# Kernel tuning notes

Measured on AMD Instinct MI355X. Metric: run time of the kernel, lower is better.

Reference implementation:

```python
import jax, jax.numpy as jnp
import numpy as np

H1, H, OUT, T = 512, 2048, 1024, 4096

def setup_inputs() -> dict:
    key = jax.random.key(0)
    ks = jax.random.split(key, 20)
    s = 0.02
    return {
        "input": jax.random.normal(ks[0], (1, OUT), jnp.float32),
        "hidden": jax.random.normal(ks[1], (1, 1, H), jnp.float32) * 0.1,
        "encoder_outputs": jax.random.normal(ks[2], (T, H), jnp.float32),
        "prenet_w": jax.random.normal(ks[3], (H1, OUT), jnp.float32) * s,
        "prenet_b": jnp.zeros((H1,), jnp.float32),
        "prenet2_w": jax.random.normal(ks[4], (H, H1), jnp.float32) * s,
        "prenet2_b": jnp.zeros((H,), jnp.float32),
        "attn1_w": jax.random.normal(ks[5], (H, H), jnp.float32) * s,
        "attn2_w": jax.random.normal(ks[6], (H, H), jnp.float32) * s,
        "attn3_w": jax.random.normal(ks[7], (1, H), jnp.float32) * s,
        "gru_w_ih": jax.random.normal(ks[8], (3 * H, 2 * H), jnp.float32) * s,
        "gru_w_hh": jax.random.normal(ks[9], (3 * H, H), jnp.float32) * s,
        "gru_b_ih": jnp.zeros((3 * H,), jnp.float32),
        "gru_b_hh": jnp.zeros((3 * H,), jnp.float32),
        "lin_w": jax.random.normal(ks[10], (OUT, H), jnp.float32) * s,
        "lin_b": jnp.zeros((OUT,), jnp.float32),
    }

def reference(input, hidden, encoder_outputs, prenet_w, prenet_b, prenet2_w,
              prenet2_b, attn1_w, attn2_w, attn3_w, gru_w_ih, gru_w_hh,
              gru_b_ih, gru_b_hh, lin_w, lin_b):
    # prenet MLP (dropout in eval mode = identity)
    em6 = jax.nn.relu(jax.nn.relu(input @ prenet_w.T + prenet_b) @ prenet2_w.T + prenet2_b)  # [1,H]
    # Bahdanau additive attention
    way = em6 @ attn1_w.T                                 # [1,H]
    uah = encoder_outputs @ attn2_w.T                     # [T,H]
    beta = jnp.tanh(way + uah)                            # [T,H] (broadcast = expand_as)
    gamma = beta @ attn3_w.T                              # [T,1]
    attn_weights = jax.nn.softmax(gamma.T, axis=1)        # [1,T]
    attn_applied = attn_weights @ encoder_outputs         # [1,H]
    # single-step GRU (PyTorch gate order: r, z, n)
    x = jnp.concatenate([em6, attn_applied], axis=1)      # [1,2H]
    h0 = hidden[0]                                        # [1,H]
    gi = x @ gru_w_ih.T + gru_b_ih                        # [1,3H]
    gh = h0 @ gru_w_hh.T + gru_b_hh                       # [1,3H]
    i_r, i_z, i_n = jnp.split(gi, 3, axis=1)
    h_r, h_z, h_n = jnp.split(gh, 3, axis=1)
    r = jax.nn.sigmoid(i_r + h_r)
    z = jax.nn.sigmoid(i_z + h_z)
    n = jnp.tanh(i_n + r * h_n)
    h_new = (1.0 - z) * n + z * h0                        # [1,H]
    out = jax.nn.softmax(h_new @ lin_w.T + lin_b, axis=1) # [1,OUT]
    return out, h_new[None], attn_weights
```

## Files before the change

### kernel.cpp

```cpp
#include <hip/hip_runtime.h>
#include <hip/hip_bf16.h>

typedef __bf16 bf16x8 __attribute__((ext_vector_type(8)));
typedef __bf16 bf16x4 __attribute__((ext_vector_type(4)));
typedef float f32x4 __attribute__((ext_vector_type(4)));

#define H1 512
#define H 2048
#define OUTN 1024
#define T 4096

__global__ __launch_bounds__(256) void matvec_k(
    const float* __restrict__ W, const float* __restrict__ x,
    const float* __restrict__ b, float* __restrict__ out,
    int R, int K, int relu)
{
    int row = blockIdx.x * 4 + (threadIdx.x >> 6);
    int lane = threadIdx.x & 63;
    if (row >= R) return;
    const float* Wr = W + (size_t)row * K;
    float s = 0.f;
    for (int k = lane * 4; k < K; k += 256) {
        float4 w4 = *(const float4*)(Wr + k);
        float4 x4 = *(const float4*)(x + k);
        s += w4.x * x4.x + w4.y * x4.y + w4.z * x4.z + w4.w * x4.w;
    }
    #pragma unroll
    for (int m = 32; m; m >>= 1) s += __shfl_xor(s, m, 64);
    if (lane == 0) {
        if (b) s += b[row];
        if (relu) s = fmaxf(s, 0.f);
        out[row] = s;
    }
}

__global__ __launch_bounds__(256) void cvt_sw_k(
    const float* __restrict__ E, const float* __restrict__ W2,
    __bf16* __restrict__ dst)
{
    int c = blockIdx.x * 256 + threadIdx.x;
    int row = c >> 8;
    int kc = c & 255;
    const float* src = (row < T) ? (E + (size_t)row * H + kc * 8)
                                 : (W2 + (size_t)(row - T) * H + kc * 8);
    float4 a = *(const float4*)src;
    float4 b = *(const float4*)(src + 4);
    bf16x8 v = {(__bf16)a.x, (__bf16)a.y, (__bf16)a.z, (__bf16)a.w,
                (__bf16)b.x, (__bf16)b.y, (__bf16)b.z, (__bf16)b.w};
    int grp = kc >> 3, cc = kc & 7;
    int sw = cc ^ (row & 7);
    *(bf16x8*)(dst + (size_t)row * H + grp * 64 + sw * 8) = v;
}

__global__ __launch_bounds__(256, 4) void gamma_gemm5(
    const __bf16* __restrict__ Asw,
    const __bf16* __restrict__ Bsw,
    const float* __restrict__ way, const float* __restrict__ a3,
    float* __restrict__ gamma)
{
    __shared__ __attribute__((aligned(16))) __bf16 As[128][64];
    __shared__ __attribute__((aligned(16))) __bf16 Bs[64][64];
    __shared__ float wayS[64], a3S[64];

    const int tb = blockIdx.x, hb = blockIdx.y;
    const int tid = threadIdx.x, lane = tid & 63, wid = tid >> 6;
    const int wr = wid >> 1, wc = wid & 1;
    if (tid < 64) { wayS[tid] = way[hb * 64 + tid]; a3S[tid] = a3[hb * 64 + tid]; }

    const int K = 2048;
    const __bf16* Ap = Asw + (size_t)(tb * 128) * K;
    const __bf16* Bp = Bsw + (size_t)(hb * 64) * K;

    f32x4 acc[4][2] = {};
    const int rl = lane & 15;
    const int kg = (lane >> 4) * 8;

    for (int t = 0; t < 32; ++t) {
        const int k0 = t * 64;
        #pragma unroll
        for (int j = 0; j < 4; ++j) {
            int c = tid + j * 256;
            int row_ = c >> 3, cc_ = c & 7;
            const __bf16* sA_ = Ap + (size_t)row_ * K + k0 + cc_ * 8;
            __builtin_amdgcn_global_load_lds(
                (const __attribute__((address_space(1))) void*)sA_,
                (__attribute__((address_space(3))) void*)((char*)&As[0][0] + c * 16),
                16, 0, 0);
        }
        #pragma unroll
        for (int j = 0; j < 2; ++j) {
            int c = tid + j * 256;
            int row_ = c >> 3, cc_ = c & 7;
            const __bf16* sB_ = Bp + (size_t)row_ * K + k0 + cc_ * 8;
            __builtin_amdgcn_global_load_lds(
                (const __attribute__((address_space(1))) void*)sB_,
                (__attribute__((address_space(3))) void*)((char*)&Bs[0][0] + c * 16),
                16, 0, 0);
        }
        __syncthreads();
        #pragma unroll
        for (int kk = 0; kk < 2; ++kk) {
            bf16x8 af[4], bfm[2];
            const int kb = (kg + kk * 32) * 2;
            #pragma unroll
            for (int mi = 0; mi < 4; ++mi) {
                int r_ = wr * 64 + mi * 16 + rl;
                af[mi] = *(const bf16x8*)((const char*)&As[0][0] + r_ * 128 + (kb ^ ((r_ & 7) << 4)));
            }
            #pragma unroll
            for (int ni = 0; ni < 2; ++ni) {
                int r_ = wc * 32 + ni * 16 + rl;
                bfm[ni] = *(const bf16x8*)((const char*)&Bs[0][0] + r_ * 128 + (kb ^ ((r_ & 7) << 4)));
            }
            #pragma unroll
            for (int mi = 0; mi < 4; ++mi)
                #pragma unroll
                for (int ni = 0; ni < 2; ++ni)
                    acc[mi][ni] = __builtin_amdgcn_mfma_f32_16x16x32_bf16(
                        af[mi], bfm[ni], acc[mi][ni], 0, 0, 0);
        }
        __syncthreads();
    }

    const int rg = lane >> 4;
    #pragma unroll
    for (int mi = 0; mi < 4; ++mi) {
        float sr[4] = {0.f, 0.f, 0.f, 0.f};
        #pragma unroll
        for (int ni = 0; ni < 2; ++ni) {
            int h = wc * 32 + ni * 16 + rl;
            float wh = wayS[h];
            float ah = a3S[h];
            #pragma unroll
            for (int r = 0; r < 4; ++r)
                sr[r] += tanhf(wh + acc[mi][ni][r]) * ah;
        }
        #pragma unroll
        for (int m = 1; m < 16; m <<= 1) {
            #pragma unroll
            for (int r = 0; r < 4; ++r)
                sr[r] += __shfl_xor(sr[r], m, 64);
        }
        if (rl == 0) {
            int t = tb * 128 + wr * 64 + mi * 16 + rg * 4;
            #pragma unroll
            for (int r = 0; r < 4; ++r)
                atomicAdd(&gamma[t + r], sr[r]);
        }
    }
}

#define BM 128
#define BN 128
#define BK 32
#define LSTR 40

__global__ __launch_bounds__(256) void gamma_gemm(
    const float* __restrict__ E, const float* __restrict__ W2,
    const float* __restrict__ way, const float* __restrict__ a3,
    float* __restrict__ gamma)
{
    __shared__ __bf16 As[BM][LSTR];
    __shared__ __bf16 Bs[BN][LSTR];
    __shared__ float wayS[BN];
    __shared__ float a3S[BN];

    const int tb = blockIdx.x, hb = blockIdx.y;
    const int tid = threadIdx.x, lane = tid & 63, wid = tid >> 6;
    const int wr = wid >> 1, wc = wid & 1;
    if (tid < BN) { wayS[tid] = way[hb * BN + tid]; a3S[tid] = a3[hb * BN + tid]; }

    f32x4 acc[4][4] = {};
    const int K = 2048;
    const float* Ep  = E  + (size_t)(tb * BM) * K;
    const float* W2p = W2 + (size_t)(hb * BN) * K;
    const int rl = lane & 15;
    const int kg = (lane >> 4) * 8;

    for (int k0 = 0; k0 < K; k0 += BK) {
        __syncthreads();
        #pragma unroll
        for (int i = 0; i < 4; ++i) {
            int c = tid + i * 256;
            int row = c >> 3;
            int col = (c & 7) * 4;
            float4 va = *(const float4*)(Ep + (size_t)row * K + k0 + col);
            bf16x4 pa = {(__bf16)va.x, (__bf16)va.y, (__bf16)va.z, (__bf16)va.w};
            *(bf16x4*)&As[row][col] = pa;
            float4 vb = *(const float4*)(W2p + (size_t)row * K + k0 + col);
            bf16x4 pb = {(__bf16)vb.x, (__bf16)vb.y, (__bf16)vb.z, (__bf16)vb.w};
            *(bf16x4*)&Bs[row][col] = pb;
        }
        __syncthreads();
        bf16x8 af[4], bfr[4];
        #pragma unroll
        for (int mi = 0; mi < 4; ++mi)
            af[mi] = *(const bf16x8*)&As[wr * 64 + mi * 16 + rl][kg];
        #pragma unroll
        for (int ni = 0; ni < 4; ++ni)
            bfr[ni] = *(const bf16x8*)&Bs[wc * 64 + ni * 16 + rl][kg];
        #pragma unroll
        for (int mi = 0; mi < 4; ++mi)
            #pragma unroll
            for (int ni = 0; ni < 4; ++ni)
                acc[mi][ni] = __builtin_amdgcn_mfma_f32_16x16x32_bf16(
                    af[mi], bfr[ni], acc[mi][ni], 0, 0, 0);
    }

    const int rg = lane >> 4;
    #pragma unroll
    for (int mi = 0; mi < 4; ++mi) {
        float sr[4] = {0.f, 0.f, 0.f, 0.f};
        #pragma unroll
        for (int ni = 0; ni < 4; ++ni) {
            int h = wc * 64 + ni * 16 + rl;
            float wh = wayS[h];
            float ah = a3S[h];
            #pragma unroll
            for (int r = 0; r < 4; ++r)
                sr[r] += tanhf(wh + acc[mi][ni][r]) * ah;
        }
        #pragma unroll
        for (int m = 1; m < 16; m <<= 1) {
            #pragma unroll
            for (int r = 0; r < 4; ++r)
                sr[r] += __shfl_xor(sr[r], m, 64);
        }
        if (rl == 0) {
            int t = tb * BM + wr * 64 + mi * 16 + rg * 4;
            #pragma unroll
            for (int r = 0; r < 4; ++r)
                atomicAdd(&gamma[t + r], sr[r]);
        }
    }
}

__global__ __launch_bounds__(1024) void softmax_k(
    const float* __restrict__ in, float* __restrict__ out, int n)
{
    __shared__ float sred[16];
    __shared__ float sbc;
    int tid = threadIdx.x;

    float m = -3.4e38f;
    for (int i = tid; i < n; i += 1024) m = fmaxf(m, in[i]);
    #pragma unroll
    for (int s = 32; s; s >>= 1) m = fmaxf(m, __shfl_xor(m, s, 64));
    if ((tid & 63) == 0) sred[tid >> 6] = m;
    __syncthreads();
    if (tid == 0) {
        float mm = sred[0];
        for (int i = 1; i < 16; ++i) mm = fmaxf(mm, sred[i]);
        sbc = mm;
    }
    __syncthreads();
    float mx = sbc;

    float s = 0.f;
    for (int i = tid; i < n; i += 1024) s += expf(in[i] - mx);
    #pragma unroll
    for (int sh = 32; sh; sh >>= 1) s += __shfl_xor(s, sh, 64);
    if ((tid & 63) == 0) sred[tid >> 6] = s;
    __syncthreads();
    if (tid == 0) {
        float ss = 0.f;
        for (int i = 0; i < 16; ++i) ss += sred[i];
        sbc = ss;
    }
    __syncthreads();
    float inv = 1.f / sbc;
    for (int i = tid; i < n; i += 1024) out[i] = expf(in[i] - mx) * inv;
}

__global__ __launch_bounds__(256) void attn_apply_k(
    const float* __restrict__ E, const float* __restrict__ w,
    float* __restrict__ outacc)
{
    int tid = threadIdx.x;
    int t0 = blockIdx.x * 32;
    float a[8] = {0.f, 0.f, 0.f, 0.f, 0.f, 0.f, 0.f, 0.f};
    for (int t = t0; t < t0 + 32; ++t) {
        float wt = w[t];
        const float* Er = E + (size_t)t * H;
        #pragma unroll
        for (int j = 0; j < 8; ++j)
            a[j] += wt * Er[tid + 256 * j];
    }
    #pragma unroll
    for (int j = 0; j < 8; ++j)
        atomicAdd(&outacc[tid + 256 * j], a[j]);
}

__global__ __launch_bounds__(256) void gru_combine_k(
    const float* __restrict__ gi, const float* __restrict__ gh,
    const float* __restrict__ h0, float* __restrict__ hout)
{
    int h = blockIdx.x * 256 + threadIdx.x;
    float ir = gi[h], iz = gi[H + h], in_ = gi[2 * H + h];
    float hr = gh[h], hz = gh[H + h], hn = gh[2 * H + h];
    float r = 1.f / (1.f + expf(-(ir + hr)));
    float z = 1.f / (1.f + expf(-(iz + hz)));
    float n = tanhf(in_ + r * hn);
    hout[h] = (1.f - z) * n + z * h0[h];
}

extern "C" void kernel_launch(void* const* d_in, const int* in_sizes, int n_in,
                              void* d_out, int out_size, void* d_ws, size_t ws_size,
                              hipStream_t stream)
{
    const float* input    = (const float*)d_in[0];
    const float* hidden   = (const float*)d_in[1];
    const float* enc      = (const float*)d_in[2];
    const float* prenet_w = (const float*)d_in[3];
    const float* prenet_b = (const float*)d_in[4];
    const float* prenet2_w= (const float*)d_in[5];
    const float* prenet2_b= (const float*)d_in[6];
    const float* attn1_w  = (const float*)d_in[7];
    const float* attn2_w  = (const float*)d_in[8];
    const float* attn3_w  = (const float*)d_in[9];
    const float* gru_w_ih = (const float*)d_in[10];
    const float* gru_w_hh = (const float*)d_in[11];
    const float* gru_b_ih = (const float*)d_in[12];
    const float* gru_b_hh = (const float*)d_in[13];
    const float* lin_w    = (const float*)d_in[14];
    const float* lin_b    = (const float*)d_in[15];

    float* out = (float*)d_out;
    float* h_new = out + OUTN;
    float* attn_w = out + OUTN + H;

    float* ws = (float*)d_ws;
    float* w_h1     = ws;
    float* w_way    = w_h1 + 512;
    float* w_gamma  = w_way + H;
    float* w_x      = w_gamma + T;
    float* w_gi     = w_x + 2 * H;
    float* w_gh     = w_gi + 3 * H;
    float* w_logits = w_gh + 3 * H;

    const size_t BF_OFF = 131072;
    const size_t BF_BYTES = (size_t)(T + H) * H * sizeof(__bf16);
    bool fast = (ws_size >= BF_OFF + BF_BYTES);
    __bf16* bfE  = (__bf16*)((char*)d_ws + BF_OFF);
    __bf16* bfW2 = bfE + (size_t)T * H;

    hipMemsetAsync(w_gamma, 0, T * sizeof(float), stream);
    hipMemsetAsync(w_x + H, 0, H * sizeof(float), stream);

    if (fast)
        cvt_sw_k<<<(T + H) * (H / 8) / 256, 256, 0, stream>>>(enc, attn2_w, bfE);

    matvec_k<<<H1 / 4, 256, 0, stream>>>(prenet_w, input, prenet_b, w_h1, H1, OUTN, 1);
    matvec_k<<<H / 4, 256, 0, stream>>>(prenet2_w, w_h1, prenet2_b, w_x, H, H1, 1);
    matvec_k<<<H / 4, 256, 0, stream>>>(attn1_w, w_x, nullptr, w_way, H, H, 0);

    if (fast)
        gamma_gemm5<<<dim3(T / 128, H / 64), 256, 0, stream>>>(bfE, bfW2, w_way, attn3_w, w_gamma);
    else
        gamma_gemm<<<dim3(T / BM, H / BN), 256, 0, stream>>>(enc, attn2_w, w_way, attn3_w, w_gamma);

    softmax_k<<<1, 1024, 0, stream>>>(w_gamma, attn_w, T);
    attn_apply_k<<<T / 32, 256, 0, stream>>>(enc, attn_w, w_x + H);
    matvec_k<<<(3 * H) / 4, 256, 0, stream>>>(gru_w_ih, w_x, gru_b_ih, w_gi, 3 * H, 2 * H, 0);
    matvec_k<<<(3 * H) / 4, 256, 0, stream>>>(gru_w_hh, hidden, gru_b_hh, w_gh, 3 * H, H, 0);
    gru_combine_k<<<H / 256, 256, 0, stream>>>(w_gi, w_gh, hidden, h_new);
    matvec_k<<<OUTN / 4, 256, 0, stream>>>(lin_w, h_new, lin_b, w_logits, OUTN, H, 0);
    softmax_k<<<1, 1024, 0, stream>>>(w_logits, out, OUTN);
}
```

Before: 133.0 us.

## Load encoder A-fragments directly from global into registers, skip LDS staging

The gamma GEMM no longer stages the encoder tile in shared memory. Each wave now owns 32 rows and reads its A fragments straight from global memory into registers, while only the W2 tile goes through LDS. The conversion kernel stops swizzling encoder rows to match. This removes LDS traffic and a large shared buffer, but it trades away cross-wave reuse of B (each wave now computes all 64 columns) and exposes global load latency inside the k loop.

```diff
diff --git a/kernel.cpp b/kernel.cpp
--- a/kernel.cpp
+++ b/kernel.cpp
@@ -48,45 +48,33 @@
     bf16x8 v = {(__bf16)a.x, (__bf16)a.y, (__bf16)a.z, (__bf16)a.w,
                 (__bf16)b.x, (__bf16)b.y, (__bf16)b.z, (__bf16)b.w};
     int grp = kc >> 3, cc = kc & 7;
-    int sw = cc ^ (row & 7);
+    int sw = (row < T) ? cc : (cc ^ (row & 7));
     *(bf16x8*)(dst + (size_t)row * H + grp * 64 + sw * 8) = v;
 }
 
-__global__ __launch_bounds__(256, 4) void gamma_gemm5(
-    const __bf16* __restrict__ Asw,
+__global__ __launch_bounds__(256, 4) void gamma_gemm6(
+    const __bf16* __restrict__ Ebf,
     const __bf16* __restrict__ Bsw,
     const float* __restrict__ way, const float* __restrict__ a3,
     float* __restrict__ gamma)
 {
-    __shared__ __attribute__((aligned(16))) __bf16 As[128][64];
     __shared__ __attribute__((aligned(16))) __bf16 Bs[64][64];
     __shared__ float wayS[64], a3S[64];
 
     const int tb = blockIdx.x, hb = blockIdx.y;
     const int tid = threadIdx.x, lane = tid & 63, wid = tid >> 6;
-    const int wr = wid >> 1, wc = wid & 1;
     if (tid < 64) { wayS[tid] = way[hb * 64 + tid]; a3S[tid] = a3[hb * 64 + tid]; }
 
     const int K = 2048;
-    const __bf16* Ap = Asw + (size_t)(tb * 128) * K;
-    const __bf16* Bp = Bsw + (size_t)(hb * 64) * K;
-
-    f32x4 acc[4][2] = {};
     const int rl = lane & 15;
     const int kg = (lane >> 4) * 8;
+    const __bf16* Arow = Ebf + (size_t)(tb * 128 + wid * 32 + rl) * K + kg;
+    const __bf16* Bp = Bsw + (size_t)(hb * 64) * K;
+
+    f32x4 acc[2][4] = {};
 
     for (int t = 0; t < 32; ++t) {
         const int k0 = t * 64;
-        #pragma unroll
-        for (int j = 0; j < 4; ++j) {
-            int c = tid + j * 256;
-            int row_ = c >> 3, cc_ = c & 7;
-            const __bf16* sA_ = Ap + (size_t)row_ * K + k0 + cc_ * 8;
-            __builtin_amdgcn_global_load_lds(
-                (const __attribute__((address_space(1))) void*)sA_,
-                (__attribute__((address_space(3))) void*)((char*)&As[0][0] + c * 16),
-                16, 0, 0);
-        }
         #pragma unroll
         for (int j = 0; j < 2; ++j) {
             int c = tid + j * 256;
@@ -97,38 +85,41 @@
                 (__attribute__((address_space(3))) void*)((char*)&Bs[0][0] + c * 16),
                 16, 0, 0);
         }
+        bf16x8 af[2][2];
+        #pragma unroll
+        for (int mi = 0; mi < 2; ++mi)
+            #pragma unroll
+            for (int kk = 0; kk < 2; ++kk)
+                af[mi][kk] = *(const bf16x8*)(Arow + (size_t)mi * 16 * K + k0 + kk * 32);
+
         __syncthreads();
+
         #pragma unroll
         for (int kk = 0; kk < 2; ++kk) {
-            bf16x8 af[4], bfm[2];
+            bf16x8 bfm[4];
             const int kb = (kg + kk * 32) * 2;
             #pragma unroll
-            for (int mi = 0; mi < 4; ++mi) {
-                int r_ = wr * 64 + mi * 16 + rl;
-                af[mi] = *(const bf16x8*)((const char*)&As[0][0] + r_ * 128 + (kb ^ ((r_ & 7) << 4)));
-            }
-            #pragma unroll
-            for (int ni = 0; ni < 2; ++ni) {
-                int r_ = wc * 32 + ni * 16 + rl;
+            for (int ni = 0; ni < 4; ++ni) {
+                int r_ = ni * 16 + rl;
                 bfm[ni] = *(const bf16x8*)((const char*)&Bs[0][0] + r_ * 128 + (kb ^ ((r_ & 7) << 4)));
             }
             #pragma unroll
-            for (int mi = 0; mi < 4; ++mi)
+            for (int mi = 0; mi < 2; ++mi)
                 #pragma unroll
-                for (int ni = 0; ni < 2; ++ni)
+                for (int ni = 0; ni < 4; ++ni)
                     acc[mi][ni] = __builtin_amdgcn_mfma_f32_16x16x32_bf16(
-                        af[mi], bfm[ni], acc[mi][ni], 0, 0, 0);
+                        af[mi][kk], bfm[ni], acc[mi][ni], 0, 0, 0);
         }
         __syncthreads();
     }
 
     const int rg = lane >> 4;
     #pragma unroll
-    for (int mi = 0; mi < 4; ++mi) {
+    for (int mi = 0; mi < 2; ++mi) {
         float sr[4] = {0.f, 0.f, 0.f, 0.f};
         #pragma unroll
-        for (int ni = 0; ni < 2; ++ni) {
-            int h = wc * 32 + ni * 16 + rl;
+        for (int ni = 0; ni < 4; ++ni) {
+            int h = ni * 16 + rl;
             float wh = wayS[h];
             float ah = a3S[h];
             #pragma unroll
@@ -142,7 +133,7 @@
                 sr[r] += __shfl_xor(sr[r], m, 64);
         }
         if (rl == 0) {
-            int t = tb * 128 + wr * 64 + mi * 16 + rg * 4;
+            int t = tb * 128 + wid * 32 + mi * 16 + rg * 4;
             #pragma unroll
             for (int r = 0; r < 4; ++r)
                 atomicAdd(&gamma[t + r], sr[r]);
@@ -355,7 +346,7 @@
     matvec_k<<<H / 4, 256, 0, stream>>>(attn1_w, w_x, nullptr, w_way, H, H, 0);
 
     if (fast)
-        gamma_gemm5<<<dim3(T / 128, H / 64), 256, 0, stream>>>(bfE, bfW2, w_way, attn3_w, w_gamma);
+        gamma_gemm6<<<dim3(T / 128, H / 64), 256, 0, stream>>>(bfE, bfW2, w_way, attn3_w, w_gamma);
     else
         gamma_gemm<<<dim3(T / BM, H / BN), 256, 0, stream>>>(enc, attn2_w, w_way, attn3_w, w_gamma);
 
```

New measurement: 160.0 us. +20.3%, slower.
